# Kernel tuning notes

Hardware: AMD Instinct MI355X
Metric: run time of the kernel (lower is better)

Reference implementation:

```python
import jax, jax.numpy as jnp
import numpy as np
from jax import lax

N_BINS = 32


def _comp_hist(dose, masks_ncv, num_voxels, n_bins):
    # dose: [N,1,D,H,W]  masks_ncv: [N,C,V]  num_voxels: [N,C]
    bw = 1.0 / n_bins
    N = dose.shape[0]
    d = dose.reshape(N, -1)  # [N,V] (C==1)
    bins = (jnp.arange(n_bins, dtype=d.dtype) * bw)  # bin edges i*bin_width

    def body(_, b):
        sig = jax.nn.sigmoid((d - b) / bw)              # [N,V]
        num = jnp.einsum('nv,ncv->c', sig, masks_ncv)   # summed over batch too (faithful to torch dim=(0,2,3,4))
        return None, num

    _, nums = lax.scan(body, None, bins)                # [B,C]
    # hist[:, i] = num / num_voxels broadcasts [C] over [N,C]
    hist = nums[None, :, :] / num_voxels[:, None, :]    # [N,B,C]
    return hist


def setup_inputs() -> dict:
    key = jax.random.key(0)
    k1, k2, k3 = jax.random.split(key, 3)
    shape = (2, 1, 128, 128, 128)
    predicted_dose = jax.random.uniform(k1, shape, jnp.float32)
    target_dose = jax.random.uniform(k2, shape, jnp.float32)
    structure_masks = jax.random.randint(k3, (2, 128, 128, 128, 10), 0, 2).astype(jnp.float32)
    return {"predicted_dose": predicted_dose, "target_dose": target_dose,
            "structure_masks": structure_masks}


def reference(predicted_dose, target_dose, structure_masks):
    N = predicted_dose.shape[0]
    # permute (0,4,1,2,3): [N,D,H,W,C] -> [N,C,D,H,W], then flatten spatial dims
    m = jnp.transpose(structure_masks, (0, 4, 1, 2, 3))
    C = m.shape[1]
    masks_ncv = m.reshape(N, C, -1)                    # [N,C,V]
    num_voxels = jnp.sum(masks_ncv, axis=2) + 1.0      # [N,C]
    ph = _comp_hist(predicted_dose, masks_ncv, num_voxels, N_BINS)
    th = _comp_hist(target_dose, masks_ncv, num_voxels, N_BINS)
    return jnp.mean((ph - th) ** 2) / N
```

## Files before the change

kernel.cpp:

```cpp
#include <hip/hip_runtime.h>

typedef __attribute__((ext_vector_type(8))) short short8;
typedef __attribute__((ext_vector_type(4))) float f32x4;
typedef __attribute__((ext_vector_type(4))) int int4v;

#define CHUNK 512
#define NBINS 32
#define NCLS  10
#define NREP  8

__device__ __forceinline__ float asf(unsigned int u) { return __builtin_bit_cast(float, u); }
__device__ __forceinline__ unsigned int asu(float f) { return __builtin_bit_cast(unsigned int, f); }

__global__ __launch_bounds__(256) void dvh_main(
    const float* __restrict__ pred, const float* __restrict__ targ,
    const float* __restrict__ mask, float* __restrict__ gD, float* __restrict__ gN,
    int chunksPerN)
{
    __shared__ float2 sE[CHUNK];
    __shared__ unsigned short mT[16 * 512];

    const int tid  = threadIdx.x;
    const int lane = tid & 63;
    const int w    = tid >> 6;
    const int n15  = lane & 15;
    const int g    = lane >> 4;

    const int chunk = blockIdx.x;
    const size_t vbase = (size_t)chunk * CHUNK;

    float2 p = ((const float2*)(pred + vbase))[tid];
    float2 t = ((const float2*)(targ + vbase))[tid];
    uint4 mv[5];
    {
        const uint4* m4g = (const uint4*)(mask + vbase * NCLS);
        #pragma unroll
        for (int k = 0; k < 5; ++k) mv[k] = m4g[k * 256 + tid];
    }

    #pragma unroll
    for (int i = 0; i < 12; ++i) mT[10 * 512 + i * 256 + tid] = 0;

    const float K1 = __expf((float)n15);
    const float K2 = K1 * 8886110.5f;

    *(float4*)&sE[2 * tid] = make_float4(__expf(-32.f * p.x), __expf(-32.f * t.x),
                                         __expf(-32.f * p.y), __expf(-32.f * t.y));
    #pragma unroll
    for (int k = 0; k < 5; ++k) {
        int f = (k * 256 + tid) * 4;
        unsigned int e[4] = {mv[k].x, mv[k].y, mv[k].z, mv[k].w};
        #pragma unroll
        for (int q = 0; q < 4; ++q) {
            int v = (f + q) / 10;
            int c = (f + q) - v * 10;
            mT[c * 512 + (((v >> 3) ^ (c & 7)) << 3) + (v & 7)] =
                (unsigned short)(e[q] >> 16);
        }
    }
    __syncthreads();

    f32x4 accH1 = {0,0,0,0}, accL1 = {0,0,0,0};
    f32x4 accH2 = {0,0,0,0}, accL2 = {0,0,0,0};
    f32x4 cnt   = {0,0,0,0};
    short8 ones;
    #pragma unroll
    for (int i = 0; i < 8; ++i) ones[i] = (short)0x3F80;

    #pragma unroll
    for (int st = 0; st < 4; ++st) {
        const int vb = (w * 4 + st) * 32;
        const int v0 = vb + g * 8;
        short8 fb = *(const short8*)&mT[n15 * 512 + (((v0 >> 3) ^ (n15 & 7)) << 3)];
        const float4* e4 = (const float4*)&sE[v0];

        int uh1[4], ul1[4], uh2[4], ul2[4];
        #pragma unroll
        for (int j = 0; j < 4; ++j) {
            float4 q = e4[j];
            float dea = q.y - q.x, deb = q.w - q.z;
            float pa = fmaf(q.x, K1, 1.f) * fmaf(q.y, K1, 1.f);
            float pb = fmaf(q.z, K1, 1.f) * fmaf(q.w, K1, 1.f);
            float sa = dea * K1 * __builtin_amdgcn_rcpf(pa);
            float sb = deb * K1 * __builtin_amdgcn_rcpf(pb);
            unsigned ua = asu(sa), ub = asu(sb);
            uh1[j] = (int)((ua >> 16) | (ub & 0xffff0000u));
            float la = sa - asf(ua & 0xffff0000u);
            float lb = sb - asf(ub & 0xffff0000u);
            unsigned lo1;
            asm("v_cvt_pk_bf16_f32 %0, %1, %2" : "=v"(lo1) : "v"(la), "v"(lb));
            ul1[j] = (int)lo1;
            float pc = fmaf(q.x, K2, 1.f) * fmaf(q.y, K2, 1.f);
            float pd = fmaf(q.z, K2, 1.f) * fmaf(q.w, K2, 1.f);
            float sc = dea * K2 * __builtin_amdgcn_rcpf(pc);
            float sd = deb * K2 * __builtin_amdgcn_rcpf(pd);
            unsigned uc = asu(sc), ud = asu(sd);
            uh2[j] = (int)((uc >> 16) | (ud & 0xffff0000u));
            float lc = sc - asf(uc & 0xffff0000u);
            float ld = sd - asf(ud & 0xffff0000u);
            unsigned lo2;
            asm("v_cvt_pk_bf16_f32 %0, %1, %2" : "=v"(lo2) : "v"(lc), "v"(ld));
            ul2[j] = (int)lo2;
        }
        int4v th1 = {uh1[0], uh1[1], uh1[2], uh1[3]};
        int4v tl1 = {ul1[0], ul1[1], ul1[2], ul1[3]};
        int4v th2 = {uh2[0], uh2[1], uh2[2], uh2[3]};
        int4v tl2 = {ul2[0], ul2[1], ul2[2], ul2[3]};
        short8 A1h = __builtin_bit_cast(short8, th1);
        short8 A1l = __builtin_bit_cast(short8, tl1);
        short8 A2h = __builtin_bit_cast(short8, th2);
        short8 A2l = __builtin_bit_cast(short8, tl2);

        accH1 = __builtin_amdgcn_mfma_f32_16x16x32_bf16(A1h, fb, accH1, 0, 0, 0);
        accL1 = __builtin_amdgcn_mfma_f32_16x16x32_bf16(A1l, fb, accL1, 0, 0, 0);
        accH2 = __builtin_amdgcn_mfma_f32_16x16x32_bf16(A2h, fb, accH2, 0, 0, 0);
        accL2 = __builtin_amdgcn_mfma_f32_16x16x32_bf16(A2l, fb, accL2, 0, 0, 0);
        cnt   = __builtin_amdgcn_mfma_f32_16x16x32_bf16(ones, fb, cnt,   0, 0, 0);
    }
    __syncthreads();

    float* red  = (float*)mT;
    float* redN = red + 1280;

    f32x4 d1 = accH1 + accL1;
    f32x4 d2 = accH2 + accL2;
    if (n15 < NCLS) {
        #pragma unroll
        for (int r = 0; r < 4; ++r) {
            int b1 = g * 4 + r;
            red[(w * 32 + b1) * NCLS + n15]      = d1[r];
            red[(w * 32 + 16 + b1) * NCLS + n15] = d2[r];
        }
    }
    if (lane < NCLS) redN[w * NCLS + lane] = cnt[0];
    __syncthreads();

    const int rep = chunk & (NREP - 1);
    float* gDr = gD + rep * (NBINS * NCLS);
    float* gNr = gN + rep * (2 * NCLS);
    const int nsel = (chunk < chunksPerN) ? 0 : 1;

    for (int i = tid; i < NBINS * NCLS; i += 256) {
        float s = red[i] + red[320 + i] + red[640 + i] + red[960 + i];
        atomicAdd(&gDr[i], s);
    }
    if (tid < NCLS) {
        float s = redN[tid] + redN[10 + tid] + redN[20 + tid] + redN[30 + tid];
        atomicAdd(&gNr[nsel * NCLS + tid], s);
    }
}

__global__ __launch_bounds__(512) void dvh_final(
    const float* __restrict__ gD, const float* __restrict__ gN, float* __restrict__ out)
{
    __shared__ float red[512];
    int t = threadIdx.x;
    float v = 0.f;
    if (t < NBINS * NCLS) {
        int c = t % NCLS;
        float nv0 = 1.f, nv1 = 1.f, d = 0.f;
        #pragma unroll
        for (int r = 0; r < NREP; ++r) {
            d   += gD[r * (NBINS * NCLS) + t];
            nv0 += gN[r * (2 * NCLS) + c];
            nv1 += gN[r * (2 * NCLS) + NCLS + c];
        }
        float w = 1.f / (nv0 * nv0) + 1.f / (nv1 * nv1);
        v = d * d * w;
    }
    red[t] = v;
    __syncthreads();
    for (int s = 256; s > 0; s >>= 1) {
        if (t < s) red[t] += red[t + s];
        __syncthreads();
    }
    if (t == 0) out[0] = red[0] * (1.f / 1280.f);
}

extern "C" void kernel_launch(void* const* d_in, const int* in_sizes, int n_in,
                              void* d_out, int out_size, void* d_ws, size_t ws_size,
                              hipStream_t stream) {
    const float* pred = (const float*)d_in[0];
    const float* targ = (const float*)d_in[1];
    const float* mask = (const float*)d_in[2];
    float* gD = (float*)d_ws;
    float* gN = (float*)((char*)d_ws + NREP * 320 * 4);

    hipMemsetAsync(d_ws, 0, NREP * (320 + 20) * 4, stream);

    int totalVox    = in_sizes[0];
    int chunksTotal = totalVox / CHUNK;
    int chunksPerN  = chunksTotal / 2;

    dvh_main<<<chunksTotal, 256, 0, stream>>>(pred, targ, mask, gD, gN, chunksPerN);
    dvh_final<<<1, 512, 0, stream>>>(gD, gN, (float*)d_out);
}
```

Baseline: 59.83 us.

## Halve chunk size, drop shared-memory reduction for direct per-wave atomics, share reciprocals

```diff
diff --git a/kernel.cpp b/kernel.cpp
--- a/kernel.cpp
+++ b/kernel.cpp
@@ -4,21 +4,21 @@
 typedef __attribute__((ext_vector_type(4))) float f32x4;
 typedef __attribute__((ext_vector_type(4))) int int4v;
 
-#define CHUNK 512
+#define CHUNK 256
 #define NBINS 32
 #define NCLS  10
-#define NREP  8
+#define NREP  16
 
 __device__ __forceinline__ float asf(unsigned int u) { return __builtin_bit_cast(float, u); }
 __device__ __forceinline__ unsigned int asu(float f) { return __builtin_bit_cast(unsigned int, f); }
 
-__global__ __launch_bounds__(256) void dvh_main(
+__global__ __launch_bounds__(128) void dvh_main(
     const float* __restrict__ pred, const float* __restrict__ targ,
     const float* __restrict__ mask, float* __restrict__ gD, float* __restrict__ gN,
     int chunksPerN)
 {
     __shared__ float2 sE[CHUNK];
-    __shared__ unsigned short mT[16 * 512];
+    __shared__ unsigned short mT[16 * CHUNK];
 
     const int tid  = threadIdx.x;
     const int lane = tid & 63;
@@ -35,11 +35,14 @@
     {
         const uint4* m4g = (const uint4*)(mask + vbase * NCLS);
         #pragma unroll
-        for (int k = 0; k < 5; ++k) mv[k] = m4g[k * 256 + tid];
+        for (int k = 0; k < 5; ++k) mv[k] = m4g[k * 128 + tid];
     }
 
-    #pragma unroll
-    for (int i = 0; i < 12; ++i) mT[10 * 512 + i * 256 + tid] = 0;
+    {
+        unsigned int* z = (unsigned int*)&mT[10 * CHUNK];
+        #pragma unroll
+        for (int i = 0; i < 6; ++i) z[i * 128 + tid] = 0;
+    }
 
     const float K1 = __expf((float)n15);
     const float K2 = K1 * 8886110.5f;
@@ -48,13 +51,13 @@
                                          __expf(-32.f * p.y), __expf(-32.f * t.y));
     #pragma unroll
     for (int k = 0; k < 5; ++k) {
-        int f = (k * 256 + tid) * 4;
+        int f = (k * 128 + tid) * 4;
         unsigned int e[4] = {mv[k].x, mv[k].y, mv[k].z, mv[k].w};
         #pragma unroll
         for (int q = 0; q < 4; ++q) {
             int v = (f + q) / 10;
             int c = (f + q) - v * 10;
-            mT[c * 512 + (((v >> 3) ^ (c & 7)) << 3) + (v & 7)] =
+            mT[c * CHUNK + (((v >> 3) ^ (c & 7)) << 3) + (v & 7)] =
                 (unsigned short)(e[q] >> 16);
         }
     }
@@ -71,7 +74,7 @@
     for (int st = 0; st < 4; ++st) {
         const int vb = (w * 4 + st) * 32;
         const int v0 = vb + g * 8;
-        short8 fb = *(const short8*)&mT[n15 * 512 + (((v0 >> 3) ^ (n15 & 7)) << 3)];
+        short8 fb = *(const short8*)&mT[n15 * CHUNK + (((v0 >> 3) ^ (n15 & 7)) << 3)];
         const float4* e4 = (const float4*)&sE[v0];
 
         int uh1[4], ul1[4], uh2[4], ul2[4];
@@ -79,28 +82,34 @@
         for (int j = 0; j < 4; ++j) {
             float4 q = e4[j];
             float dea = q.y - q.x, deb = q.w - q.z;
-            float pa = fmaf(q.x, K1, 1.f) * fmaf(q.y, K1, 1.f);
-            float pb = fmaf(q.z, K1, 1.f) * fmaf(q.w, K1, 1.f);
-            float sa = dea * K1 * __builtin_amdgcn_rcpf(pa);
-            float sb = deb * K1 * __builtin_amdgcn_rcpf(pb);
-            unsigned ua = asu(sa), ub = asu(sb);
-            uh1[j] = (int)((ua >> 16) | (ub & 0xffff0000u));
-            float la = sa - asf(ua & 0xffff0000u);
-            float lb = sb - asf(ub & 0xffff0000u);
-            unsigned lo1;
-            asm("v_cvt_pk_bf16_f32 %0, %1, %2" : "=v"(lo1) : "v"(la), "v"(lb));
-            ul1[j] = (int)lo1;
-            float pc = fmaf(q.x, K2, 1.f) * fmaf(q.y, K2, 1.f);
-            float pd = fmaf(q.z, K2, 1.f) * fmaf(q.w, K2, 1.f);
-            float sc = dea * K2 * __builtin_amdgcn_rcpf(pc);
-            float sd = deb * K2 * __builtin_amdgcn_rcpf(pd);
-            unsigned uc = asu(sc), ud = asu(sd);
-            uh2[j] = (int)((uc >> 16) | (ud & 0xffff0000u));
-            float lc = sc - asf(uc & 0xffff0000u);
-            float ld = sd - asf(ud & 0xffff0000u);
-            unsigned lo2;
-            asm("v_cvt_pk_bf16_f32 %0, %1, %2" : "=v"(lo2) : "v"(lc), "v"(ld));
-            ul2[j] = (int)lo2;
+            {
+                float pra = fmaf(q.x, K1, 1.f) * fmaf(q.y, K1, 1.f);
+                float prb = fmaf(q.z, K1, 1.f) * fmaf(q.w, K1, 1.f);
+                float rD  = __builtin_amdgcn_rcpf(pra * prb);
+                float sa  = (dea * K1) * (prb * rD);
+                float sb  = (deb * K1) * (pra * rD);
+                unsigned ua = asu(sa), ub = asu(sb);
+                uh1[j] = (int)((ua >> 16) | (ub & 0xffff0000u));
+                float la = sa - asf(ua & 0xffff0000u);
+                float lb = sb - asf(ub & 0xffff0000u);
+                unsigned lo1;
+                asm("v_cvt_pk_bf16_f32 %0, %1, %2" : "=v"(lo1) : "v"(la), "v"(lb));
+                ul1[j] = (int)lo1;
+            }
+            {
+                float pra = fmaf(q.x, K2, 1.f) * fmaf(q.y, K2, 1.f);
+                float prb = fmaf(q.z, K2, 1.f) * fmaf(q.w, K2, 1.f);
+                float rD  = __builtin_amdgcn_rcpf(pra * prb);
+                float sa  = (dea * K2) * (prb * rD);
+                float sb  = (deb * K2) * (pra * rD);
+                unsigned ua = asu(sa), ub = asu(sb);
+                uh2[j] = (int)((ua >> 16) | (ub & 0xffff0000u));
+                float la = sa - asf(ua & 0xffff0000u);
+                float lb = sb - asf(ub & 0xffff0000u);
+                unsigned lo2;
+                asm("v_cvt_pk_bf16_f32 %0, %1, %2" : "=v"(lo2) : "v"(la), "v"(lb));
+                ul2[j] = (int)lo2;
+            }
         }
         int4v th1 = {uh1[0], uh1[1], uh1[2], uh1[3]};
         int4v tl1 = {ul1[0], ul1[1], ul1[2], ul1[3]};
@@ -117,10 +126,11 @@
         accL2 = __builtin_amdgcn_mfma_f32_16x16x32_bf16(A2l, fb, accL2, 0, 0, 0);
         cnt   = __builtin_amdgcn_mfma_f32_16x16x32_bf16(ones, fb, cnt,   0, 0, 0);
     }
-    __syncthreads();
 
-    float* red  = (float*)mT;
-    float* redN = red + 1280;
+    const int rep = chunk & (NREP - 1);
+    float* gDr = gD + rep * (NBINS * NCLS);
+    float* gNr = gN + rep * (2 * NCLS);
+    const int nsel = (chunk < chunksPerN) ? 0 : 1;
 
     f32x4 d1 = accH1 + accL1;
     f32x4 d2 = accH2 + accL2;
@@ -128,26 +138,11 @@
         #pragma unroll
         for (int r = 0; r < 4; ++r) {
             int b1 = g * 4 + r;
-            red[(w * 32 + b1) * NCLS + n15]      = d1[r];
-            red[(w * 32 + 16 + b1) * NCLS + n15] = d2[r];
+            atomicAdd(&gDr[b1 * NCLS + n15],        d1[r]);
+            atomicAdd(&gDr[(16 + b1) * NCLS + n15], d2[r]);
         }
     }
-    if (lane < NCLS) redN[w * NCLS + lane] = cnt[0];
-    __syncthreads();
-
-    const int rep = chunk & (NREP - 1);
-    float* gDr = gD + rep * (NBINS * NCLS);
-    float* gNr = gN + rep * (2 * NCLS);
-    const int nsel = (chunk < chunksPerN) ? 0 : 1;
-
-    for (int i = tid; i < NBINS * NCLS; i += 256) {
-        float s = red[i] + red[320 + i] + red[640 + i] + red[960 + i];
-        atomicAdd(&gDr[i], s);
-    }
-    if (tid < NCLS) {
-        float s = redN[tid] + redN[10 + tid] + redN[20 + tid] + redN[30 + tid];
-        atomicAdd(&gNr[nsel * NCLS + tid], s);
-    }
+    if (lane < NCLS) atomicAdd(&gNr[nsel * NCLS + lane], cnt[0]);
 }
 
 __global__ __launch_bounds__(512) void dvh_final(
@@ -184,14 +179,14 @@
     const float* targ = (const float*)d_in[1];
     const float* mask = (const float*)d_in[2];
     float* gD = (float*)d_ws;
-    float* gN = (float*)((char*)d_ws + NREP * 320 * 4);
+    float* gN = (float*)((char*)d_ws + NREP * NBINS * NCLS * 4);
 
-    hipMemsetAsync(d_ws, 0, NREP * (320 + 20) * 4, stream);
+    hipMemsetAsync(d_ws, 0, NREP * (NBINS * NCLS + 2 * NCLS) * 4, stream);
 
     int totalVox    = in_sizes[0];
     int chunksTotal = totalVox / CHUNK;
     int chunksPerN  = chunksTotal / 2;
 
-    dvh_main<<<chunksTotal, 256, 0, stream>>>(pred, targ, mask, gD, gN, chunksPerN);
+    dvh_main<<<chunksTotal, 128, 0, stream>>>(pred, targ, mask, gD, gN, chunksPerN);
     dvh_final<<<1, 512, 0, stream>>>(gD, gN, (float*)d_out);
 }
```

After: 190.7 us. 3.19x slower.

## Share one reciprocal across voxel pairs and widen atomic replication to 64

Applied to the files above, without the earlier changes.

```diff
diff --git a/kernel.cpp b/kernel.cpp
--- a/kernel.cpp
+++ b/kernel.cpp
@@ -7,7 +7,7 @@
 #define CHUNK 512
 #define NBINS 32
 #define NCLS  10
-#define NREP  8
+#define NREP  64
 
 __device__ __forceinline__ float asf(unsigned int u) { return __builtin_bit_cast(float, u); }
 __device__ __forceinline__ unsigned int asu(float f) { return __builtin_bit_cast(unsigned int, f); }
@@ -79,28 +79,34 @@
         for (int j = 0; j < 4; ++j) {
             float4 q = e4[j];
             float dea = q.y - q.x, deb = q.w - q.z;
-            float pa = fmaf(q.x, K1, 1.f) * fmaf(q.y, K1, 1.f);
-            float pb = fmaf(q.z, K1, 1.f) * fmaf(q.w, K1, 1.f);
-            float sa = dea * K1 * __builtin_amdgcn_rcpf(pa);
-            float sb = deb * K1 * __builtin_amdgcn_rcpf(pb);
-            unsigned ua = asu(sa), ub = asu(sb);
-            uh1[j] = (int)((ua >> 16) | (ub & 0xffff0000u));
-            float la = sa - asf(ua & 0xffff0000u);
-            float lb = sb - asf(ub & 0xffff0000u);
-            unsigned lo1;
-            asm("v_cvt_pk_bf16_f32 %0, %1, %2" : "=v"(lo1) : "v"(la), "v"(lb));
-            ul1[j] = (int)lo1;
-            float pc = fmaf(q.x, K2, 1.f) * fmaf(q.y, K2, 1.f);
-            float pd = fmaf(q.z, K2, 1.f) * fmaf(q.w, K2, 1.f);
-            float sc = dea * K2 * __builtin_amdgcn_rcpf(pc);
-            float sd = deb * K2 * __builtin_amdgcn_rcpf(pd);
-            unsigned uc = asu(sc), ud = asu(sd);
-            uh2[j] = (int)((uc >> 16) | (ud & 0xffff0000u));
-            float lc = sc - asf(uc & 0xffff0000u);
-            float ld = sd - asf(ud & 0xffff0000u);
-            unsigned lo2;
-            asm("v_cvt_pk_bf16_f32 %0, %1, %2" : "=v"(lo2) : "v"(lc), "v"(ld));
-            ul2[j] = (int)lo2;
+            {
+                float pra = fmaf(q.x, K1, 1.f) * fmaf(q.y, K1, 1.f);
+                float prb = fmaf(q.z, K1, 1.f) * fmaf(q.w, K1, 1.f);
+                float rD  = __builtin_amdgcn_rcpf(pra * prb);
+                float sa  = (dea * K1) * (prb * rD);
+                float sb  = (deb * K1) * (pra * rD);
+                unsigned ua = asu(sa), ub = asu(sb);
+                uh1[j] = (int)((ua >> 16) | (ub & 0xffff0000u));
+                float la = sa - asf(ua & 0xffff0000u);
+                float lb = sb - asf(ub & 0xffff0000u);
+                unsigned lo1;
+                asm("v_cvt_pk_bf16_f32 %0, %1, %2" : "=v"(lo1) : "v"(la), "v"(lb));
+                ul1[j] = (int)lo1;
+            }
+            {
+                float pra = fmaf(q.x, K2, 1.f) * fmaf(q.y, K2, 1.f);
+                float prb = fmaf(q.z, K2, 1.f) * fmaf(q.w, K2, 1.f);
+                float rD  = __builtin_amdgcn_rcpf(pra * prb);
+                float sa  = (dea * K2) * (prb * rD);
+                float sb  = (deb * K2) * (pra * rD);
+                unsigned ua = asu(sa), ub = asu(sb);
+                uh2[j] = (int)((ua >> 16) | (ub & 0xffff0000u));
+                float la = sa - asf(ua & 0xffff0000u);
+                float lb = sb - asf(ub & 0xffff0000u);
+                unsigned lo2;
+                asm("v_cvt_pk_bf16_f32 %0, %1, %2" : "=v"(lo2) : "v"(la), "v"(lb));
+                ul2[j] = (int)lo2;
+            }
         }
         int4v th1 = {uh1[0], uh1[1], uh1[2], uh1[3]};
         int4v tl1 = {ul1[0], ul1[1], ul1[2], ul1[3]};
@@ -159,7 +165,6 @@
     if (t < NBINS * NCLS) {
         int c = t % NCLS;
         float nv0 = 1.f, nv1 = 1.f, d = 0.f;
-        #pragma unroll
         for (int r = 0; r < NREP; ++r) {
             d   += gD[r * (NBINS * NCLS) + t];
             nv0 += gN[r * (2 * NCLS) + c];
@@ -184,9 +189,9 @@
     const float* targ = (const float*)d_in[1];
     const float* mask = (const float*)d_in[2];
     float* gD = (float*)d_ws;
-    float* gN = (float*)((char*)d_ws + NREP * 320 * 4);
-
-    hipMemsetAsync(d_ws, 0, NREP * (320 + 20) * 4, stream);
+    float* gN = (float*)((char*)d_ws + NREP * NBINS * NCLS * 4);
+
+    hipMemsetAsync(d_ws, 0, NREP * (NBINS * NCLS + 2 * NCLS) * 4, stream);
 
     int totalVox    = in_sizes[0];
     int chunksTotal = totalVox / CHUNK;
```

New measurement: 77.58 us. +29.7%, slower.
